# Optimization experiments

Hardware: AMD Instinct MI355X
Metric: run time of the kernel (lower is better)

The kernel has to match this reference:

```python
import jax, jax.numpy as jnp
import numpy as np


def setup_inputs() -> dict:
    key = jax.random.key(0)
    ks = jax.random.split(key, 5)
    B, S, E, H, D = 4, 2048, 1024, 16, 64
    sc = 1.0 / np.sqrt(E)
    x = jax.random.normal(ks[0], (B, S, E), dtype=jnp.float32)
    Wq = jax.random.normal(ks[1], (H, E, D), dtype=jnp.float32) * sc
    Wk = jax.random.normal(ks[2], (H, E, D), dtype=jnp.float32) * sc
    Wv = jax.random.normal(ks[3], (H, E, D), dtype=jnp.float32) * sc
    Wo = jax.random.normal(ks[4], (E, E), dtype=jnp.float32) * sc
    bo = jnp.zeros((E,), dtype=jnp.float32)
    return {"x": x, "Wq": Wq, "Wk": Wk, "Wv": Wv, "Wo": Wo, "bo": bo}


def reference(x, Wq, Wk, Wv, Wo, bo):
    # x: [B,S,E]; Wq/Wk/Wv: [H,E,D]; Wo: [E,E]; bo: [E]
    B, S, E = x.shape
    H, _, D = Wq.shape
    q = jnp.einsum('bse,hed->bhsd', x, Wq)
    k = jnp.einsum('bse,hed->bhsd', x, Wk)
    v = jnp.einsum('bse,hed->bhsd', x, Wv)
    scale = jnp.asarray(D, x.dtype) ** -0.5
    att = jnp.einsum('bhsd,bhtd->bhst', q, k) * scale  # [B,H,S,S]
    causal = jnp.tril(jnp.ones((S, S), dtype=bool))
    att = jnp.where(causal, att, jnp.asarray(-jnp.inf, att.dtype))
    att = jax.nn.softmax(att, axis=-1)
    out = jnp.einsum('bhst,bhtd->bhsd', att, v)  # [B,H,S,D]
    # concat heads in order (head dim-major on last axis), then project
    out = out.transpose(0, 2, 1, 3).reshape(B, S, H * D)
    return out @ Wo.T + bo
```

## Files before the change

kernel.cpp:

```cpp
#include <hip/hip_runtime.h>
#include <hip/hip_bf16.h>

#define BB 4
#define SS 2048
#define EE 1024
#define HH 16
#define DD 64
#define MM (BB*SS)
#define HD (HH*DD)
#define NQKV (3*HD)

typedef __bf16 bf16_t;
typedef __bf16 bf16x4 __attribute__((ext_vector_type(4)));
typedef __bf16 bf16x8 __attribute__((ext_vector_type(8)));
typedef float f32x4 __attribute__((ext_vector_type(4)));

#define MFMA16(a,b,c) __builtin_amdgcn_mfma_f32_16x16x32_bf16(a,b,c,0,0,0)
#define NEG_INF (-__builtin_huge_valf())
#define QSCALE 0.1803368801111204f
#define CSHIFT 12.0f

__device__ __forceinline__ void gload_lds16(const void* g, void* l) {
  __builtin_amdgcn_global_load_lds((const __attribute__((address_space(1))) unsigned int*)g,
                                   (__attribute__((address_space(3))) unsigned int*)l,
                                   16, 0, 0);
}

#define SBAR() __builtin_amdgcn_s_barrier()
#define SCHB() __builtin_amdgcn_sched_barrier(0)
#define VMCNT6 do { asm volatile("s_waitcnt vmcnt(6)" ::: "memory"); } while(0)
#define VMCNT2 do { asm volatile("s_waitcnt vmcnt(2)" ::: "memory"); } while(0)
#define VMCNT0 do { asm volatile("s_waitcnt vmcnt(0)" ::: "memory"); } while(0)

__global__ __launch_bounds__(256)
void k_f32_to_bf16(const float* __restrict__ in, bf16_t* __restrict__ out, int n8) {
  int i = blockIdx.x*256 + threadIdx.x;
  if (i >= n8) return;
  const float4* p = reinterpret_cast<const float4*>(in) + (size_t)i*2;
  float4 a = p[0], b = p[1];
  bf16x8 o;
  o[0]=(bf16_t)a.x; o[1]=(bf16_t)a.y; o[2]=(bf16_t)a.z; o[3]=(bf16_t)a.w;
  o[4]=(bf16_t)b.x; o[5]=(bf16_t)b.y; o[6]=(bf16_t)b.z; o[7]=(bf16_t)b.w;
  *reinterpret_cast<bf16x8*>(out + (size_t)i*8) = o;
}

__global__ __launch_bounds__(256)
void k_conv_wqkv(const float* __restrict__ Wq, const float* __restrict__ Wk,
                 const float* __restrict__ Wv, bf16_t* __restrict__ Wt) {
  __shared__ float t[64][65];
  int wh = blockIdx.x;
  int which = wh >> 4, h = wh & 15;
  int e0 = blockIdx.y * 64;
  const float* W = (which==0) ? Wq : (which==1) ? Wk : Wv;
  const float* src = W + (size_t)h*EE*DD;
  int r = threadIdx.x >> 6, c = threadIdx.x & 63;
  #pragma unroll
  for (int i = 0; i < 16; ++i) {
    int e = i*4 + r;
    t[e][c] = src[(size_t)(e0+e)*DD + c];
  }
  __syncthreads();
  bf16_t* dst = Wt + (size_t)(which*HD + h*DD)*EE;
  #pragma unroll
  for (int i = 0; i < 16; ++i) {
    int d = i*4 + r;
    dst[(size_t)d*EE + e0 + c] = (bf16_t)t[c][d];
  }
}

#define NKT 16
template<int EPI, int NTX>
__global__ __launch_bounds__(512, 1)
void k_gemm8(const bf16_t* __restrict__ Ag, const bf16_t* __restrict__ Bg0,
             bf16_t* __restrict__ Qp, bf16_t* __restrict__ Kp, bf16_t* __restrict__ Vtp,
             const float* __restrict__ bias, float* __restrict__ Cout) {
  __shared__ __align__(16) bf16_t Ab[3][128*64];
  __shared__ __align__(16) bf16_t Bb[3][256*64];

  int orig = blockIdx.x;
  int xcd = orig & 7, lidx = orig >> 3;
  int tileY = xcd*8 + (lidx & 7);
  int tileX = lidx >> 3;
  int n0 = tileX * 256, m0 = tileY * 128;

  int tid = threadIdx.x;
  int lane = tid & 63, w = tid >> 6;
  int wr = w >> 2, wc = w & 3;
  int lr = lane & 15, lg = lane >> 4;

  const bf16_t* Bg = Bg0 + (size_t)n0 * EE;

  int r3 = tid >> 3;
  int gch = (tid & 7) ^ (r3 & 7);
  int ldsb = w * 1024;

#define STAGE_A(buf, kt) do { \
    const bf16_t* g_ = Ag + (size_t)(m0 + r3)*EE + (kt)*64 + gch*8; \
    char* l_ = (char*)Ab[buf] + ldsb; \
    gload_lds16(g_, l_); \
    gload_lds16(g_ + (size_t)64*EE, l_ + 8192); \
  } while(0)
#define STAGE_B(buf, kt, half) do { \
    const bf16_t* g_ = Bg + (size_t)((half)*128 + r3)*EE + (kt)*64 + gch*8; \
    char* l_ = (char*)Bb[buf] + (half)*16384 + ldsb; \
    gload_lds16(g_, l_); \
    gload_lds16(g_ + (size_t)64*EE, l_ + 8192); \
  } while(0)

  int sA = lr & 7;
  unsigned aoff[2] = { (unsigned)((wr*64 + lr)*128 + ((lg     ^ sA) << 4)),
                       (unsigned)((wr*64 + lr)*128 + (((4+lg) ^ sA) << 4)) };
  unsigned boff[2] = { (unsigned)((wc*64 + lr)*128 + ((lg     ^ sA) << 4)),
                       (unsigned)((wc*64 + lr)*128 + (((4+lg) ^ sA) << 4)) };

  f32x4 acc[4][4];
  #pragma unroll
  for (int i=0;i<4;i++)
    #pragma unroll
    for (int j=0;j<4;j++) acc[i][j] = (f32x4){0.f,0.f,0.f,0.f};
  bf16x8 af[4], bq[4];

#define PHASE2(buf, kh, STAGE_STMT, WAITV) do { \
    _Pragma("unroll") for (int mf_=0; mf_<4; ++mf_) \
      af[mf_] = *reinterpret_cast<const bf16x8*>((const char*)Ab[buf] + aoff[kh] + mf_*2048); \
    _Pragma("unroll") for (int nf_=0; nf_<4; ++nf_) \
      bq[nf_] = *reinterpret_cast<const bf16x8*>((const char*)Bb[buf] + boff[kh] + nf_*2048); \
    STAGE_STMT; \
    SBAR(); \
    asm volatile("s_waitcnt lgkmcnt(0)" ::: "memory"); \
    SCHB(); \
    __builtin_amdgcn_s_setprio(1); \
    _Pragma("unroll") for (int mf_=0; mf_<4; ++mf_) \
      _Pragma("unroll") for (int nf_=0; nf_<4; ++nf_) \
        acc[mf_][nf_] = MFMA16(af[mf_], bq[nf_], acc[mf_][nf_]); \
    __builtin_amdgcn_s_setprio(0); \
    WAITV; \
    SBAR(); \
    SCHB(); \
  } while(0)

  STAGE_A(0, 0); STAGE_B(0, 0, 0); STAGE_B(0, 0, 1);
  STAGE_A(1, 1); STAGE_B(1, 1, 0); STAGE_B(1, 1, 1);
  VMCNT6;
  SBAR();
  SCHB();

  #pragma unroll
  for (int t = 0; t < NKT; ++t) {
    int cur = t % 3, pre = (t+2) % 3;
    bool more = (t+2 < NKT);
    PHASE2(cur, 0, if (more) STAGE_A(pre, t+2), (void)0);
    PHASE2(cur, 1, if (more) { STAGE_B(pre, t+2, 0); STAGE_B(pre, t+2, 1); },
           { if (more) { VMCNT6; } else { VMCNT0; } });
  }
#undef PHASE2
#undef STAGE_A
#undef STAGE_B

  if (EPI == 0) {
    int which = n0 >> 10;
    if (which < 2) {
      #pragma unroll
      for (int mf=0; mf<4; ++mf) {
        #pragma unroll
        for (int nf=0; nf<4; ++nf) {
          int n = n0 + wc*64 + nf*16 + lr;
          int hd = n & 1023, h2 = hd >> 6, d = hd & 63;
          #pragma unroll
          for (int r=0;r<4;r++) {
            int m = m0 + wr*64 + mf*16 + lg*4 + r;
            int b = m >> 11, s = m & 2047;
            size_t bh = (size_t)(b*HH + h2);
            if (which == 0) Qp[(bh*SS + s)*DD + d] = (bf16_t)(acc[mf][nf][r] * QSCALE);
            else            Kp[(bh*SS + s)*DD + d] = (bf16_t)acc[mf][nf][r];
          }
        }
      }
    } else {
      #pragma unroll
      for (int mf=0; mf<4; ++mf) {
        #pragma unroll
        for (int nf=0; nf<4; ++nf) {
          int n = n0 + wc*64 + nf*16 + lr;
          int hd = n & 1023, h2 = hd >> 6, d = hd & 63;
          int m = m0 + wr*64 + mf*16 + lg*4;
          int b = m >> 11, s = m & 2047;
          size_t bh = (size_t)(b*HH + h2);
          bf16x4 vv;
          vv[0] = (bf16_t)acc[mf][nf][0];
          vv[1] = (bf16_t)acc[mf][nf][1];
          vv[2] = (bf16_t)acc[mf][nf][2];
          vv[3] = (bf16_t)acc[mf][nf][3];
          *reinterpret_cast<bf16x4*>(Vtp + (bh*DD + d)*SS + s) = vv;
        }
      }
    }
  } else {
    float bv[4];
    #pragma unroll
    for (int nf=0;nf<4;nf++) bv[nf] = bias[n0 + wc*64 + nf*16 + lr];
    #pragma unroll
    for (int mf=0; mf<4; ++mf)
      #pragma unroll
      for (int nf=0; nf<4; ++nf) {
        int n = n0 + wc*64 + nf*16 + lr;
        #pragma unroll
        for (int r=0;r<4;r++) {
          int m = m0 + wr*64 + mf*16 + lg*4 + r;
          Cout[(size_t)m*HD + n] = acc[mf][nf][r] + bv[nf];
        }
      }
  }
}

__global__ __launch_bounds__(512)
void k_attn(const bf16_t* __restrict__ Q, const bf16_t* __restrict__ K,
            const bf16_t* __restrict__ Vt, bf16_t* __restrict__ AO) {
  __shared__ __align__(16) bf16_t Ks[3][64*64];
  __shared__ __align__(16) bf16_t Vs[3][64*64];

  int id = blockIdx.x;
  int m8 = id & 7, d8 = id >> 3;
  int bh = m8*8 + (d8 >> 3);
  int u  = d8 & 7;

  int tid = threadIdx.x, lane = tid & 63, w = tid >> 6;
  int lr = lane & 15, lg = lane >> 4;
  const bf16_t* Qb = Q  + (size_t)bh * SS * DD;
  const bf16_t* Kp = K  + (size_t)bh * SS * DD;
  const bf16_t* Vp = Vt + (size_t)bh * DD * SS;
  int b = bh >> 4, h = bh & 15;

  int srow = tid >> 3;
  int gchunk = (tid & 7) ^ (srow & 7);

  bf16x8 onesf;
  #pragma unroll
  for (int i=0;i<8;i++) onesf[i] = (bf16_t)1.0f;

#define STAGE_KV(t, buf) do { \
    int kv0_ = (t)*64; \
    gload_lds16(Kp + (size_t)(kv0_ + srow)*DD + gchunk*8, (char*)Ks[buf] + w*1024); \
    gload_lds16(Vp + (size_t)srow*SS + kv0_ + gchunk*8,   (char*)Vs[buf] + w*1024); \
  } while(0)

  for (int ph = 0; ph < 2; ++ph) {
    int p = ph ? (15 - u) : u;
    int nt = 2*p + 2;
    int qrow0 = p*128 + w*16;
    int q = qrow0 + lr;

    bf16x8 qf[2];
    #pragma unroll
    for (int kk=0;kk<2;kk++)
      qf[kk] = *reinterpret_cast<const bf16x8*>(Qb + (size_t)(qrow0 + lr)*DD + kk*32 + lg*8);

    f32x4 po[4];
    #pragma unroll
    for (int i=0;i<4;i++) po[i] = (f32x4){0.f,0.f,0.f,0.f};
    f32x4 acclv = (f32x4){0.f,0.f,0.f,0.f};

    STAGE_KV(0, 0);
    STAGE_KV(1, 1);
    for (int t = 0; t < nt; ++t) {
      if (t < nt-1) { VMCNT2; } else { VMCNT0; }
      SBAR();
      SCHB();
      if (t+2 < nt) STAGE_KV(t+2, (t+2)%3);
      int kv0 = t*64;
      if (kv0 > qrow0 + 15) continue;
      int buf = t % 3;
      const bf16_t* Kb = Ks[buf];
      const bf16_t* Vb = Vs[buf];

      f32x4 sa[4];
      #pragma unroll
      for (int ct=0; ct<4; ++ct) {
        int rr = ct*16 + lr;
        int sw = rr & 7;
        bf16x8 k0 = *reinterpret_cast<const bf16x8*>(Kb + rr*64 + ((lg     ^ sw) << 3));
        bf16x8 k1 = *reinterpret_cast<const bf16x8*>(Kb + rr*64 + (((4+lg) ^ sw) << 3));
        f32x4 c = (f32x4){0.f,0.f,0.f,0.f};
        c = MFMA16(k0, qf[0], c);
        c = MFMA16(k1, qf[1], c);
        sa[ct] = c;
      }
      if (kv0 + 63 > qrow0) {
        #pragma unroll
        for (int ct=0;ct<4;ct++) {
          #pragma unroll
          for (int r=0;r<4;r++) {
            int kv = kv0 + ct*16 + lg*4 + r;
            if (kv > q) sa[ct][r] = NEG_INF;
          }
        }
      }
      bf16x8 pf[2];
      #pragma unroll
      for (int ct=0;ct<4;ct++)
        #pragma unroll
        for (int r=0;r<4;r++)
          pf[ct>>1][(ct&1)*4 + r] = (bf16_t)__builtin_amdgcn_exp2f(sa[ct][r] - CSHIFT);
      acclv = MFMA16(onesf, pf[0], acclv);
      acclv = MFMA16(onesf, pf[1], acclv);
      #pragma unroll
      for (int ctd=0; ctd<4; ++ctd) {
        int rr = ctd*16 + lr;
        int sw8 = rr & 7;
        int sub = (lg & 1) << 3;
        const char* rowb = (const char*)Vb + rr*128;
        #pragma unroll
        for (int kk=0; kk<2; ++kk) {
          int c0 = kk*4 + (lg>>1);
          bf16x4 lo = *reinterpret_cast<const bf16x4*>(rowb + (((c0     ^ sw8) << 4) | sub));
          bf16x4 hi = *reinterpret_cast<const bf16x4*>(rowb + ((((c0+2) ^ sw8) << 4) | sub));
          bf16x8 vf;
          vf[0]=lo[0]; vf[1]=lo[1]; vf[2]=lo[2]; vf[3]=lo[3];
          vf[4]=hi[0]; vf[5]=hi[1]; vf[6]=hi[2]; vf[7]=hi[3];
          po[ctd] = MFMA16(vf, pf[kk], po[ctd]);
        }
      }
    }
    SBAR();
    {
      float inv = 1.0f / acclv[0];
      bf16_t* dst = AO + (size_t)(b*SS + q)*HD + h*DD;
      #pragma unroll
      for (int ctd=0;ctd<4;ctd++) {
        bf16x4 vv;
        #pragma unroll
        for (int r=0;r<4;r++) vv[r] = (bf16_t)(po[ctd][r] * inv);
        *reinterpret_cast<bf16x4*>(dst + ctd*16 + lg*4) = vv;
      }
    }
  }
#undef STAGE_KV
}

extern "C" void kernel_launch(void* const* d_in, const int* in_sizes, int n_in,
                              void* d_out, int out_size, void* d_ws, size_t ws_size,
                              hipStream_t stream) {
  const float* x  = (const float*)d_in[0];
  const float* Wq = (const float*)d_in[1];
  const float* Wk = (const float*)d_in[2];
  const float* Wv = (const float*)d_in[3];
  const float* Wo = (const float*)d_in[4];
  const float* bo = (const float*)d_in[5];
  float* out = (float*)d_out;

  char* ws = (char*)d_ws;
  bf16_t* xb  = (bf16_t*)(ws + 0);
  bf16_t* wt  = (bf16_t*)(ws + 16777216);
  bf16_t* wob = (bf16_t*)(ws + 23068672);
  bf16_t* Qb  = (bf16_t*)(ws + 25165824);
  bf16_t* Kb  = (bf16_t*)(ws + 41943040);
  bf16_t* Vtb = (bf16_t*)(ws + 58720256);
  bf16_t* AO  = (bf16_t*)(ws + 75497472);

  k_f32_to_bf16<<<(MM*EE/8)/256, 256, 0, stream>>>(x,  xb,  MM*EE/8);
  k_f32_to_bf16<<<(EE*EE/8)/256, 256, 0, stream>>>(Wo, wob, EE*EE/8);
  dim3 gw(48, 16);
  k_conv_wqkv<<<gw, 256, 0, stream>>>(Wq, Wk, Wv, wt);

  k_gemm8<0,12><<<768, 512, 0, stream>>>(xb, wt, Qb, Kb, Vtb, nullptr, nullptr);

  k_attn<<<BB*HH*8, 512, 0, stream>>>(Qb, Kb, Vtb, AO);

  k_gemm8<1,4><<<256, 512, 0, stream>>>(AO, wob, nullptr, nullptr, nullptr, bo, out);
}
```

Before: 162.5 us.

## Retile GEMMs to 128x128x32 with occupancy 3 and pre-permute V layout

Replaces the 512-thread 128x256x64 GEMM with a 256-thread 128x128x32 tile kernel that allows three blocks per CU, doubling grid sizes for both the QKV projection and the output projection. The aim is more resident waves to hide latency, at the cost of less data reuse per tile and twice as many k-steps and barriers. Separately, the V-transpose epilogue writes sequence positions in a permuted order. This lets the attention kernel read each V fragment with one 16-byte LDS load instead of two 8-byte loads plus repacking.

```diff
diff --git a/kernel.cpp b/kernel.cpp
--- a/kernel.cpp
+++ b/kernel.cpp
@@ -28,7 +28,7 @@
 
 #define SBAR() __builtin_amdgcn_s_barrier()
 #define SCHB() __builtin_amdgcn_sched_barrier(0)
-#define VMCNT6 do { asm volatile("s_waitcnt vmcnt(6)" ::: "memory"); } while(0)
+#define VMCNT4 do { asm volatile("s_waitcnt vmcnt(4)" ::: "memory"); } while(0)
 #define VMCNT2 do { asm volatile("s_waitcnt vmcnt(2)" ::: "memory"); } while(0)
 #define VMCNT0 do { asm volatile("s_waitcnt vmcnt(0)" ::: "memory"); } while(0)
 
@@ -68,50 +68,45 @@
   }
 }
 
-#define NKT 16
 template<int EPI, int NTX>
-__global__ __launch_bounds__(512, 1)
-void k_gemm8(const bf16_t* __restrict__ Ag, const bf16_t* __restrict__ Bg0,
-             bf16_t* __restrict__ Qp, bf16_t* __restrict__ Kp, bf16_t* __restrict__ Vtp,
-             const float* __restrict__ bias, float* __restrict__ Cout) {
-  __shared__ __align__(16) bf16_t Ab[3][128*64];
-  __shared__ __align__(16) bf16_t Bb[3][256*64];
+__global__ __launch_bounds__(256, 3)
+void k_gemm32(const bf16_t* __restrict__ Ag, const bf16_t* __restrict__ Bg0,
+              bf16_t* __restrict__ Qp, bf16_t* __restrict__ Kp, bf16_t* __restrict__ Vtp,
+              const float* __restrict__ bias, float* __restrict__ Cout) {
+  __shared__ __align__(16) bf16_t Ab[3][128*32];
+  __shared__ __align__(16) bf16_t Bb[3][128*32];
 
   int orig = blockIdx.x;
   int xcd = orig & 7, lidx = orig >> 3;
   int tileY = xcd*8 + (lidx & 7);
   int tileX = lidx >> 3;
-  int n0 = tileX * 256, m0 = tileY * 128;
+  int n0 = tileX * 128, m0 = tileY * 128;
 
   int tid = threadIdx.x;
   int lane = tid & 63, w = tid >> 6;
-  int wr = w >> 2, wc = w & 3;
+  int wr = w >> 1, wc = w & 1;
   int lr = lane & 15, lg = lane >> 4;
 
   const bf16_t* Bg = Bg0 + (size_t)n0 * EE;
 
-  int r3 = tid >> 3;
-  int gch = (tid & 7) ^ (r3 & 7);
+  int r4 = tid >> 2;
+  int gch = (tid & 3) ^ ((tid >> 3) & 3);
   int ldsb = w * 1024;
 
-#define STAGE_A(buf, kt) do { \
-    const bf16_t* g_ = Ag + (size_t)(m0 + r3)*EE + (kt)*64 + gch*8; \
-    char* l_ = (char*)Ab[buf] + ldsb; \
-    gload_lds16(g_, l_); \
-    gload_lds16(g_ + (size_t)64*EE, l_ + 8192); \
+#define STAGE_A32(buf, kt) do { \
+    const bf16_t* g_ = Ag + (size_t)(m0 + r4)*EE + (kt)*32 + gch*8; \
+    gload_lds16(g_,                 (char*)Ab[buf] + ldsb); \
+    gload_lds16(g_ + (size_t)64*EE, (char*)Ab[buf] + 4096 + ldsb); \
   } while(0)
-#define STAGE_B(buf, kt, half) do { \
-    const bf16_t* g_ = Bg + (size_t)((half)*128 + r3)*EE + (kt)*64 + gch*8; \
-    char* l_ = (char*)Bb[buf] + (half)*16384 + ldsb; \
-    gload_lds16(g_, l_); \
-    gload_lds16(g_ + (size_t)64*EE, l_ + 8192); \
+#define STAGE_B32(buf, kt) do { \
+    const bf16_t* g_ = Bg + (size_t)r4*EE + (kt)*32 + gch*8; \
+    gload_lds16(g_,                 (char*)Bb[buf] + ldsb); \
+    gload_lds16(g_ + (size_t)64*EE, (char*)Bb[buf] + 4096 + ldsb); \
   } while(0)
 
-  int sA = lr & 7;
-  unsigned aoff[2] = { (unsigned)((wr*64 + lr)*128 + ((lg     ^ sA) << 4)),
-                       (unsigned)((wr*64 + lr)*128 + (((4+lg) ^ sA) << 4)) };
-  unsigned boff[2] = { (unsigned)((wc*64 + lr)*128 + ((lg     ^ sA) << 4)),
-                       (unsigned)((wc*64 + lr)*128 + (((4+lg) ^ sA) << 4)) };
+  int swA = (lr >> 1) & 3;
+  unsigned aoff = (unsigned)((wr*64 + lr)*64 + ((lg ^ swA) << 4));
+  unsigned boff = (unsigned)((wc*64 + lr)*64 + ((lg ^ swA) << 4));
 
   f32x4 acc[4][4];
   #pragma unroll
@@ -120,11 +115,11 @@
     for (int j=0;j<4;j++) acc[i][j] = (f32x4){0.f,0.f,0.f,0.f};
   bf16x8 af[4], bq[4];
 
-#define PHASE2(buf, kh, STAGE_STMT, WAITV) do { \
+#define PHASE32(buf, STAGE_STMT, WAITV) do { \
     _Pragma("unroll") for (int mf_=0; mf_<4; ++mf_) \
-      af[mf_] = *reinterpret_cast<const bf16x8*>((const char*)Ab[buf] + aoff[kh] + mf_*2048); \
+      af[mf_] = *reinterpret_cast<const bf16x8*>((const char*)Ab[buf] + aoff + mf_*1024); \
     _Pragma("unroll") for (int nf_=0; nf_<4; ++nf_) \
-      bq[nf_] = *reinterpret_cast<const bf16x8*>((const char*)Bb[buf] + boff[kh] + nf_*2048); \
+      bq[nf_] = *reinterpret_cast<const bf16x8*>((const char*)Bb[buf] + boff + nf_*1024); \
     STAGE_STMT; \
     SBAR(); \
     asm volatile("s_waitcnt lgkmcnt(0)" ::: "memory"); \
@@ -139,23 +134,23 @@
     SCHB(); \
   } while(0)
 
-  STAGE_A(0, 0); STAGE_B(0, 0, 0); STAGE_B(0, 0, 1);
-  STAGE_A(1, 1); STAGE_B(1, 1, 0); STAGE_B(1, 1, 1);
-  VMCNT6;
+  STAGE_A32(0, 0); STAGE_B32(0, 0);
+  STAGE_A32(1, 1); STAGE_B32(1, 1);
+  VMCNT4;
   SBAR();
   SCHB();
 
   #pragma unroll
-  for (int t = 0; t < NKT; ++t) {
+  for (int t = 0; t < 32; ++t) {
     int cur = t % 3, pre = (t+2) % 3;
-    bool more = (t+2 < NKT);
-    PHASE2(cur, 0, if (more) STAGE_A(pre, t+2), (void)0);
-    PHASE2(cur, 1, if (more) { STAGE_B(pre, t+2, 0); STAGE_B(pre, t+2, 1); },
-           { if (more) { VMCNT6; } else { VMCNT0; } });
-  }
-#undef PHASE2
-#undef STAGE_A
-#undef STAGE_B
+    bool more = (t+2 < 32);
+    PHASE32(cur,
+            if (more) { STAGE_A32(pre, t+2); STAGE_B32(pre, t+2); },
+            { if (more) { VMCNT4; } else { VMCNT0; } });
+  }
+#undef PHASE32
+#undef STAGE_A32
+#undef STAGE_B32
 
   if (EPI == 0) {
     int which = n0 >> 10;
@@ -185,13 +180,14 @@
           int hd = n & 1023, h2 = hd >> 6, d = hd & 63;
           int m = m0 + wr*64 + mf*16 + lg*4;
           int b = m >> 11, s = m & 2047;
+          int sp = (s & ~0x1C) | ((s & 0xC) << 1) | ((s & 0x10) >> 2);
           size_t bh = (size_t)(b*HH + h2);
           bf16x4 vv;
           vv[0] = (bf16_t)acc[mf][nf][0];
           vv[1] = (bf16_t)acc[mf][nf][1];
           vv[2] = (bf16_t)acc[mf][nf][2];
           vv[3] = (bf16_t)acc[mf][nf][3];
-          *reinterpret_cast<bf16x4*>(Vtp + (bh*DD + d)*SS + s) = vv;
+          *reinterpret_cast<bf16x4*>(Vtp + (bh*DD + d)*SS + sp) = vv;
         }
       }
     }
@@ -307,16 +303,10 @@
       for (int ctd=0; ctd<4; ++ctd) {
         int rr = ctd*16 + lr;
         int sw8 = rr & 7;
-        int sub = (lg & 1) << 3;
         const char* rowb = (const char*)Vb + rr*128;
         #pragma unroll
         for (int kk=0; kk<2; ++kk) {
-          int c0 = kk*4 + (lg>>1);
-          bf16x4 lo = *reinterpret_cast<const bf16x4*>(rowb + (((c0     ^ sw8) << 4) | sub));
-          bf16x4 hi = *reinterpret_cast<const bf16x4*>(rowb + ((((c0+2) ^ sw8) << 4) | sub));
-          bf16x8 vf;
-          vf[0]=lo[0]; vf[1]=lo[1]; vf[2]=lo[2]; vf[3]=lo[3];
-          vf[4]=hi[0]; vf[5]=hi[1]; vf[6]=hi[2]; vf[7]=hi[3];
+          bf16x8 vf = *reinterpret_cast<const bf16x8*>(rowb + (((kk*4 + lg) ^ sw8) << 4));
           po[ctd] = MFMA16(vf, pf[kk], po[ctd]);
         }
       }
@@ -362,9 +352,9 @@
   dim3 gw(48, 16);
   k_conv_wqkv<<<gw, 256, 0, stream>>>(Wq, Wk, Wv, wt);
 
-  k_gemm8<0,12><<<768, 512, 0, stream>>>(xb, wt, Qb, Kb, Vtb, nullptr, nullptr);
+  k_gemm32<0,24><<<1536, 256, 0, stream>>>(xb, wt, Qb, Kb, Vtb, nullptr, nullptr);
 
   k_attn<<<BB*HH*8, 512, 0, stream>>>(Qb, Kb, Vtb, AO);
 
-  k_gemm8<1,4><<<256, 512, 0, stream>>>(AO, wob, nullptr, nullptr, nullptr, bo, out);
-}
+  k_gemm32<1,8><<<512, 256, 0, stream>>>(AO, wob, nullptr, nullptr, nullptr, bo, out);
+}
```

Result: faster. 151.6 us (-6.7%).
